# Performance work log

Measured on AMD Instinct MI355X. Metric: run time of the kernel, lower is better.

Reference implementation:

```python
import jax, jax.numpy as jnp
import numpy as np

B, T, D = 4096, 200, 64
N_USERS, N_ITEMS = 100000, 100000


def _linear_init(k, out_dim, in_dim):
    kw, kb = jax.random.split(k)
    lim = 1.0 / np.sqrt(in_dim)
    w = jax.random.uniform(kw, (out_dim, in_dim), minval=-lim, maxval=lim, dtype=jnp.float32)
    b = jax.random.uniform(kb, (out_dim,), minval=-lim, maxval=lim, dtype=jnp.float32)
    return w, b


def setup_inputs() -> dict:
    key = jax.random.key(0)
    ks = jax.random.split(key, 16)
    gru_w_ih, gru_b_ih = _linear_init(ks[0], 3 * D, D)   # torch GRU gate order: r, z, n
    gru_w_hh, gru_b_hh = _linear_init(ks[1], 3 * D, D)
    attn_w, attn_b = _linear_init(ks[2], D, D)
    wr_w, wr_b = _linear_init(ks[3], D, 2 * D)
    wz_w, wz_b = _linear_init(ks[4], D, 2 * D)
    wh_w, wh_b = _linear_init(ks[5], D, 2 * D)
    aux_w, aux_b = _linear_init(ks[6], 1, D)
    item_emb = jax.random.normal(ks[7], (N_ITEMS + 1, D), dtype=jnp.float32)
    user_bias = jax.random.normal(ks[8], (N_USERS, 1), dtype=jnp.float32) * 0.01
    item_bias = jax.random.normal(ks[9], (N_ITEMS, 1), dtype=jnp.float32) * 0.01
    u_idx = jax.random.randint(ks[10], (B,), 0, N_USERS)
    i_idx = jax.random.randint(ks[11], (B,), 0, N_ITEMS)
    seq = jax.random.randint(ks[12], (B, T), 0, N_ITEMS + 1)
    return dict(u_idx=u_idx, i_idx=i_idx, seq=seq,
                item_emb=item_emb, user_bias=user_bias, item_bias=item_bias,
                gru_w_ih=gru_w_ih, gru_b_ih=gru_b_ih, gru_w_hh=gru_w_hh, gru_b_hh=gru_b_hh,
                attn_w=attn_w, attn_b=attn_b,
                wr_w=wr_w, wr_b=wr_b, wz_w=wz_w, wz_b=wz_b, wh_w=wh_w, wh_b=wh_b,
                aux_w=aux_w, aux_b=aux_b)


def _gru(seq_emb, w_ih, b_ih, w_hh, b_hh):
    # seq_emb: [B, T, D]. Precompute input projections for all timesteps.
    x_proj = jnp.einsum('btd,gd->btg', seq_emb, w_ih) + b_ih  # [B, T, 3D]
    x_proj = jnp.transpose(x_proj, (1, 0, 2))                 # [T, B, 3D]
    h0 = jnp.zeros((seq_emb.shape[0], D), dtype=seq_emb.dtype)

    def step(h, xp):
        gh = h @ w_hh.T + b_hh
        xr, xz, xn = jnp.split(xp, 3, axis=-1)
        hr, hz, hn = jnp.split(gh, 3, axis=-1)
        r = jax.nn.sigmoid(xr + hr)
        z = jax.nn.sigmoid(xz + hz)
        n = jnp.tanh(xn + r * hn)
        h_new = (1.0 - z) * n + z * h
        return h_new, h_new

    _, hs = jax.lax.scan(step, h0, x_proj)
    return jnp.transpose(hs, (1, 0, 2))  # [B, T, D]


def _augru(seq_emb, attn_w_t, wr_w, wr_b, wz_w, wz_b, wh_w, wh_b):
    # Split each [D, 2D] weight into x-part and h-part (input was concat([x, h])).
    wr_x, wr_h = wr_w[:, :D], wr_w[:, D:]
    wz_x, wz_h = wz_w[:, :D], wz_w[:, D:]
    wh_x, wh_h = wh_w[:, :D], wh_w[:, D:]
    xr = jnp.einsum('btd,hd->bth', seq_emb, wr_x) + wr_b  # [B, T, D]
    xz = jnp.einsum('btd,hd->bth', seq_emb, wz_x) + wz_b
    xh = jnp.einsum('btd,hd->bth', seq_emb, wh_x) + wh_b
    h0 = jnp.zeros((seq_emb.shape[0], D), dtype=seq_emb.dtype)
    inputs = (jnp.transpose(xr, (1, 0, 2)), jnp.transpose(xz, (1, 0, 2)),
              jnp.transpose(xh, (1, 0, 2)), attn_w_t.T)  # [T,B,D]x3, [T,B]

    def step(h, inp):
        xr_t, xz_t, xh_t, a_t = inp
        r = jax.nn.sigmoid(xr_t + h @ wr_h.T)
        z = jax.nn.sigmoid(xz_t + h @ wz_h.T)
        h_hat = jnp.tanh(xh_t + (r * h) @ wh_h.T)
        z = a_t[:, None] * z
        h_new = (1.0 - z) * h + z * h_hat
        return h_new, None

    h_final, _ = jax.lax.scan(step, h0, inputs)
    return h_final  # [B, D]


def reference(u_idx, i_idx, seq, item_emb, user_bias, item_bias,
              gru_w_ih, gru_b_ih, gru_w_hh, gru_b_hh, attn_w, attn_b,
              wr_w, wr_b, wz_w, wz_b, wh_w, wh_b, aux_w, aux_b):
    fm1 = user_bias[u_idx] + item_bias[i_idx]          # [B, 1]
    target_emb = item_emb[i_idx]                       # [B, D]
    seq_emb = item_emb[seq]                            # [B, T, D]

    gru_out = _gru(seq_emb, gru_w_ih, gru_b_ih, gru_w_hh, gru_b_hh)  # [B, T, D]

    target_proj = target_emb @ attn_w.T + attn_b       # [B, D]
    attn_scores = jnp.einsum('btd,bd->bt', gru_out, target_proj)
    attn_weights = jax.nn.sigmoid(attn_scores)         # [B, T]

    attn_vec = _augru(seq_emb, attn_weights, wr_w, wr_b, wz_w, wz_b, wh_w, wh_b)  # [B, D]

    aux_logits = (gru_out[:, -1, :] @ aux_w.T + aux_b)[:, 0]  # [B]
    return (fm1, attn_vec, aux_logits)
```

## Files before the change

### kernel.cpp

```cpp
#include <hip/hip_runtime.h>

typedef __bf16 bf16x8 __attribute__((ext_vector_type(8)));
typedef float f32x4 __attribute__((ext_vector_type(4)));

#define T_LEN 200
#define NB 4096

__device__ __forceinline__ f32x4 mfma16(bf16x8 a, bf16x8 b, f32x4 c) {
    return __builtin_amdgcn_mfma_f32_16x16x32_bf16(a, b, c, 0, 0, 0);
}
__device__ __forceinline__ float sigf(float x) {
    return __builtin_amdgcn_rcpf(1.0f + __expf(-x));
}
__device__ __forceinline__ float tanh_fast(float x) {
    return 1.0f - 2.0f * __builtin_amdgcn_rcpf(__expf(2.0f * x) + 1.0f);
}

__device__ __forceinline__ unsigned packRNE2(float a, float b) {
    unsigned ha = (unsigned)__builtin_bit_cast(unsigned short, (__bf16)a);
    unsigned hb = (unsigned)__builtin_bit_cast(unsigned short, (__bf16)b);
    return ha | (hb << 16);
}
__device__ __forceinline__ void publish_hi(unsigned short* hp, float v) {
    __bf16 h = (__bf16)v;
    *hp = __builtin_bit_cast(unsigned short, h);
}

struct Frag { bf16x8 hi, lo; };
__device__ __forceinline__ Frag make_frag(f32x4 a, f32x4 b) {
    Frag f;
    #pragma unroll
    for (int j = 0; j < 4; j++) {
        float v = a[j]; __bf16 h = (__bf16)v;
        f.hi[j] = h; f.lo[j] = (__bf16)(v - (float)h);
    }
    #pragma unroll
    for (int j = 0; j < 4; j++) {
        float v = b[j]; __bf16 h = (__bf16)v;
        f.hi[4 + j] = h; f.lo[4 + j] = (__bf16)(v - (float)h);
    }
    return f;
}
__device__ __forceinline__ bf16x8 load_w(const float* p) {
    f32x4 a = *(const f32x4*)p, b = *(const f32x4*)(p + 4);
    bf16x8 w;
    #pragma unroll
    for (int j = 0; j < 4; j++) { w[j] = (__bf16)a[j]; w[4 + j] = (__bf16)b[j]; }
    return w;
}

__global__ __launch_bounds__(512, 2)
void dien_fused(const int* __restrict__ u_idx, const int* __restrict__ i_idx,
                const int* __restrict__ seq, const float* __restrict__ item_emb,
                const float* __restrict__ user_bias, const float* __restrict__ item_bias,
                const float* __restrict__ gw_ih, const float* __restrict__ gb_ih,
                const float* __restrict__ gw_hh, const float* __restrict__ gb_hh,
                const float* __restrict__ attn_w, const float* __restrict__ attn_b,
                const float* __restrict__ wr_w, const float* __restrict__ wr_b,
                const float* __restrict__ wz_w, const float* __restrict__ wz_b,
                const float* __restrict__ wh_w, const float* __restrict__ wh_b,
                const float* __restrict__ aux_w, const float* __restrict__ aux_b,
                float* __restrict__ out)
{
    __shared__ int sSeq[16][T_LEN];
    __shared__ __align__(16) float sTP[16][64];
    __shared__ __align__(16) unsigned short sHGhi[16][72];
    __shared__ __align__(16) unsigned short sHAhi[16][72];
    __shared__ __align__(16) unsigned short sRHhi[16][72];
    __shared__ __align__(16) unsigned short sXhi[16][72];
    __shared__ float sScore[2][16];
    __shared__ float sParts[16][4];

    const int tid  = threadIdx.x;
    const int wave = tid >> 6;
    const int lane = tid & 63;
    const int c    = lane & 15;
    const int q    = lane >> 4;
    const bool isG = (wave < 4);
    const int wg   = wave & 3;
    const int dglob = wg * 16 + c;
    const int row0 = blockIdx.x * 16;

    for (int i = tid; i < 16 * T_LEN; i += 512) {
        int b = i / T_LEN, t = i - b * T_LEN;
        sSeq[b][t] = seq[(row0 + b) * T_LEN + t];
    }

    if (tid < 16) {
        int b = row0 + tid;
        out[b] = user_bias[u_idx[b]] + item_bias[i_idx[b]];
    }

    if (tid < 256) {
        int b  = tid >> 4;
        int d0 = (tid & 15) * 4;
        const float* erow = item_emb + (long)i_idx[row0 + b] * 64;
        float e[64];
        #pragma unroll
        for (int k4 = 0; k4 < 16; k4++) {
            f32x4 v = *(const f32x4*)(erow + k4 * 4);
            #pragma unroll
            for (int j = 0; j < 4; j++) e[k4 * 4 + j] = v[j];
        }
        #pragma unroll
        for (int dd = 0; dd < 4; dd++) {
            int d = d0 + dd;
            const float* wrow = attn_w + d * 64;
            float s = attn_b[d];
            #pragma unroll
            for (int k4 = 0; k4 < 16; k4++) {
                f32x4 wv = *(const f32x4*)(wrow + k4 * 4);
                #pragma unroll
                for (int j = 0; j < 4; j++) s += e[k4 * 4 + j] * wv[j];
            }
            sTP[b][d] = s;
        }
    }

    for (int i = tid; i < 16 * 72; i += 512) sHAhi[0][i] = 0;
    const int xrow = wg * 4 + (lane >> 4);
    const int xch  = lane & 15;
    if (isG) {
        const float* p = item_emb + (long)seq[(row0 + xrow) * T_LEN + 0] * 64 + xch * 4;
        f32x4 v = *(const f32x4*)p;
        *(uint2*)&sXhi[xrow][xch * 4] =
            make_uint2(packRNE2(v[0], v[1]), packRNE2(v[2], v[3]));
    }
    __syncthreads();

    bf16x8 W[12];
    if (isG) {
        #pragma unroll
        for (int g = 0; g < 3; g++)
            #pragma unroll
            for (int s = 0; s < 2; s++) {
                W[g * 2 + s]     = load_w(gw_ih + (g * 64 + dglob) * 64 + s * 32 + q * 8);
                W[6 + g * 2 + s] = load_w(gw_hh + (g * 64 + dglob) * 64 + s * 32 + q * 8);
            }
    } else {
        #pragma unroll
        for (int s = 0; s < 2; s++) {
            const int fo = dglob * 128 + s * 32 + q * 8;
            W[0 + s]  = load_w(wr_w + fo);
            W[2 + s]  = load_w(wr_w + fo + 64);
            W[4 + s]  = load_w(wz_w + fo);
            W[6 + s]  = load_w(wz_w + fo + 64);
            W[8 + s]  = load_w(wh_w + fo);
            W[10 + s] = load_w(wh_w + fo + 64);
        }
    }

    float bA, bB, bC, bD;
    if (isG) {
        bA = gb_ih[dglob] + gb_hh[dglob];
        bB = gb_ih[64 + dglob] + gb_hh[64 + dglob];
        bC = gb_ih[128 + dglob];
        bD = gb_hh[128 + dglob];
    } else {
        bA = wr_b[dglob];
        bB = wz_b[dglob];
        bC = wh_b[dglob];
        bD = 0.0f;
    }
    const float auxwc = aux_w[dglob];

    Frag tpB0, tpB1;
    if (isG) {
        tpB0 = make_frag(*(const f32x4*)&sTP[c][q * 8], *(const f32x4*)&sTP[c][q * 8 + 4]);
        tpB1 = make_frag(*(const f32x4*)&sTP[c][32 + q * 8], *(const f32x4*)&sTP[c][32 + q * 8 + 4]);
    }

    float hst[4] = {0.f, 0.f, 0.f, 0.f};
    bf16x8 fr0, fr1;
    #pragma unroll
    for (int j = 0; j < 8; j++) { fr0[j] = (__bf16)0.f; fr1[j] = (__bf16)0.f; }
    f32x4 aAH = {0.f, 0.f, 0.f, 0.f};
    float z_c[4] = {0.f, 0.f, 0.f, 0.f};

    f32x4 xnxt = {0.f, 0.f, 0.f, 0.f};
    if (isG) {
        int t1 = (T_LEN > 1) ? 1 : 0;
        xnxt = *(const f32x4*)(item_emb + (long)sSeq[xrow][t1] * 64 + xch * 4);
    }

    for (int t = 0; t < T_LEN; t++) {
        f32x4 xg;
        f32x4 aAR, aAZ;

        bf16x8 x0 = *(const bf16x8*)&sXhi[c][q * 8];
        bf16x8 x1 = *(const bf16x8*)&sXhi[c][32 + q * 8];

        if (isG) {
            int tn = t + 2; if (tn > T_LEN - 1) tn = T_LEN - 1;
            xg = *(const f32x4*)(item_emb + (long)sSeq[xrow][tn] * 64 + xch * 4);

            f32x4 accR = {bA, bA, bA, bA};
            accR = mfma16(x0, W[0], accR); accR = mfma16(x1, W[1], accR);
            accR = mfma16(fr0, W[6], accR); accR = mfma16(fr1, W[7], accR);
            f32x4 accZ = {bB, bB, bB, bB};
            accZ = mfma16(x0, W[2], accZ); accZ = mfma16(x1, W[3], accZ);
            accZ = mfma16(fr0, W[8], accZ); accZ = mfma16(fr1, W[9], accZ);
            f32x4 accNX = {bC, bC, bC, bC};
            accNX = mfma16(x0, W[4], accNX); accNX = mfma16(x1, W[5], accNX);
            f32x4 accNH = {bD, bD, bD, bD};
            accNH = mfma16(fr0, W[10], accNH); accNH = mfma16(fr1, W[11], accNH);

            #pragma unroll
            for (int i = 0; i < 4; i++) {
                float r = sigf(accR[i]);
                float z = sigf(accZ[i]);
                float n = tanh_fast(accNX[i] + r * accNH[i]);
                float hn = n + z * (hst[i] - n);
                hst[i] = hn;
                publish_hi(&sHGhi[q * 4 + i][dglob], hn);
            }
        } else {
            if (t > 0) {
                bf16x8 rh0 = *(const bf16x8*)&sRHhi[c][q * 8];
                bf16x8 rh1 = *(const bf16x8*)&sRHhi[c][32 + q * 8];
                aAH = mfma16(rh0, W[10], aAH); aAH = mfma16(rh1, W[11], aAH);
                #pragma unroll
                for (int i = 0; i < 4; i++) {
                    int rr = q * 4 + i;
                    float a = sScore[(t - 1) & 1][rr];
                    float hh = tanh_fast(aAH[i]);
                    float zz = a * z_c[i];
                    float hv = hst[i] + zz * (hh - hst[i]);
                    hst[i] = hv;
                    publish_hi(&sHAhi[rr][dglob], hv);
                }
            }
            aAR = (f32x4){bA, bA, bA, bA};
            aAR = mfma16(x0, W[0], aAR); aAR = mfma16(x1, W[1], aAR);
            aAZ = (f32x4){bB, bB, bB, bB};
            aAZ = mfma16(x0, W[4], aAZ); aAZ = mfma16(x1, W[5], aAZ);
            aAH = (f32x4){bC, bC, bC, bC};
            aAH = mfma16(x0, W[8], aAH); aAH = mfma16(x1, W[9], aAH);
        }

        __syncthreads();

        if (isG) {
            fr0 = *(const bf16x8*)&sHGhi[c][q * 8];
            fr1 = *(const bf16x8*)&sHGhi[c][32 + q * 8];
            f32x4 sc = {0.f, 0.f, 0.f, 0.f};
            sc = mfma16(fr0, tpB0.hi, sc); sc = mfma16(fr0, tpB0.lo, sc);
            sc = mfma16(fr1, tpB1.hi, sc); sc = mfma16(fr1, tpB1.lo, sc);
            if (wg == 0 && (c >> 2) == q) {
                int i = c & 3;
                float d = (i == 0) ? sc[0] : (i == 1) ? sc[1] : (i == 2) ? sc[2] : sc[3];
                sScore[t & 1][c] = sigf(d);
            }
            *(uint2*)&sXhi[xrow][xch * 4] =
                make_uint2(packRNE2(xnxt[0], xnxt[1]), packRNE2(xnxt[2], xnxt[3]));
            xnxt = xg;
        } else {
            bf16x8 ha0 = *(const bf16x8*)&sHAhi[c][q * 8];
            bf16x8 ha1 = *(const bf16x8*)&sHAhi[c][32 + q * 8];
            aAR = mfma16(ha0, W[2], aAR); aAR = mfma16(ha1, W[3], aAR);
            aAZ = mfma16(ha0, W[6], aAZ); aAZ = mfma16(ha1, W[7], aAZ);
            #pragma unroll
            for (int i = 0; i < 4; i++) {
                float r = sigf(aAR[i]);
                z_c[i]  = sigf(aAZ[i]);
                float rh = r * hst[i];
                publish_hi(&sRHhi[q * 4 + i][dglob], rh);
            }
        }

        __syncthreads();
    }

    if (!isG) {
        bf16x8 rh0 = *(const bf16x8*)&sRHhi[c][q * 8];
        bf16x8 rh1 = *(const bf16x8*)&sRHhi[c][32 + q * 8];
        aAH = mfma16(rh0, W[10], aAH); aAH = mfma16(rh1, W[11], aAH);
        #pragma unroll
        for (int i = 0; i < 4; i++) {
            int rr = q * 4 + i;
            float a = sScore[(T_LEN - 1) & 1][rr];
            float hh = tanh_fast(aAH[i]);
            float zz = a * z_c[i];
            float hv = hst[i] + zz * (hh - hst[i]);
            out[NB + (row0 + rr) * 64 + dglob] = hv;
        }
    }

    if (isG) {
        float pa[4];
        #pragma unroll
        for (int i = 0; i < 4; i++) pa[i] = hst[i] * auxwc;
        #pragma unroll
        for (int m = 1; m < 16; m <<= 1) {
            #pragma unroll
            for (int i = 0; i < 4; i++) pa[i] += __shfl_xor(pa[i], m, 64);
        }
        if (c == 0) {
            #pragma unroll
            for (int i = 0; i < 4; i++) sParts[q * 4 + i][wg] = pa[i];
        }
    }
    __syncthreads();
    if (tid < 16) {
        out[NB + NB * 64 + row0 + tid] =
            sParts[tid][0] + sParts[tid][1] + sParts[tid][2] + sParts[tid][3] + aux_b[0];
    }
}

extern "C" void kernel_launch(void* const* d_in, const int* in_sizes, int n_in,
                              void* d_out, int out_size, void* d_ws, size_t ws_size,
                              hipStream_t stream) {
    dien_fused<<<dim3(256), dim3(512), 0, stream>>>(
        (const int*)d_in[0],
        (const int*)d_in[1],
        (const int*)d_in[2],
        (const float*)d_in[3],
        (const float*)d_in[4],
        (const float*)d_in[5],
        (const float*)d_in[6],
        (const float*)d_in[7],
        (const float*)d_in[8],
        (const float*)d_in[9],
        (const float*)d_in[10],
        (const float*)d_in[11],
        (const float*)d_in[12],
        (const float*)d_in[13],
        (const float*)d_in[14],
        (const float*)d_in[15],
        (const float*)d_in[16],
        (const float*)d_in[17],
        (const float*)d_in[18],
        (const float*)d_in[19],
        (float*)d_out);
}
```

Baseline: 263.6 us.

## Move GRU gate math after barrier and compute attention score via shuffle partial sums

The GRU waves now issue their MFMAs before the first barrier but apply the nonlinearities and publish the hidden state after it. The GRU hidden state and input tiles are double-buffered in shared memory. The attention score is no longer an MFMA against a hi/lo split target projection. Each wave instead does fp32 dot-product partials with xor shuffles, writes four per-row partials to shared memory, and the AUGRU waves sum them and apply the sigmoid. This removes the post-barrier reload of h and the 4-MFMA score path from the critical chain, at the cost of extra shuffles and more LDS buffers.

Measured after the change: 331.9 us. 25.9% more time.

```diff
diff --git a/kernel.cpp b/kernel.cpp
--- a/kernel.cpp
+++ b/kernel.cpp
@@ -15,7 +15,6 @@
 __device__ __forceinline__ float tanh_fast(float x) {
     return 1.0f - 2.0f * __builtin_amdgcn_rcpf(__expf(2.0f * x) + 1.0f);
 }
-
 __device__ __forceinline__ unsigned packRNE2(float a, float b) {
     unsigned ha = (unsigned)__builtin_bit_cast(unsigned short, (__bf16)a);
     unsigned hb = (unsigned)__builtin_bit_cast(unsigned short, (__bf16)b);
@@ -24,22 +23,6 @@
 __device__ __forceinline__ void publish_hi(unsigned short* hp, float v) {
     __bf16 h = (__bf16)v;
     *hp = __builtin_bit_cast(unsigned short, h);
-}
-
-struct Frag { bf16x8 hi, lo; };
-__device__ __forceinline__ Frag make_frag(f32x4 a, f32x4 b) {
-    Frag f;
-    #pragma unroll
-    for (int j = 0; j < 4; j++) {
-        float v = a[j]; __bf16 h = (__bf16)v;
-        f.hi[j] = h; f.lo[j] = (__bf16)(v - (float)h);
-    }
-    #pragma unroll
-    for (int j = 0; j < 4; j++) {
-        float v = b[j]; __bf16 h = (__bf16)v;
-        f.hi[4 + j] = h; f.lo[4 + j] = (__bf16)(v - (float)h);
-    }
-    return f;
 }
 __device__ __forceinline__ bf16x8 load_w(const float* p) {
     f32x4 a = *(const f32x4*)p, b = *(const f32x4*)(p + 4);
@@ -64,11 +47,11 @@
 {
     __shared__ int sSeq[16][T_LEN];
     __shared__ __align__(16) float sTP[16][64];
-    __shared__ __align__(16) unsigned short sHGhi[16][72];
-    __shared__ __align__(16) unsigned short sHAhi[16][72];
-    __shared__ __align__(16) unsigned short sRHhi[16][72];
-    __shared__ __align__(16) unsigned short sXhi[16][72];
-    __shared__ float sScore[2][16];
+    __shared__ __align__(16) unsigned short sHG[2][16][72];
+    __shared__ __align__(16) unsigned short sHA[16][72];
+    __shared__ __align__(16) unsigned short sRH[16][72];
+    __shared__ __align__(16) unsigned short sX[2][16][72];
+    __shared__ __align__(16) float sPart[2][16][4];
     __shared__ float sParts[16][4];
 
     const int tid  = threadIdx.x;
@@ -117,13 +100,16 @@
         }
     }
 
-    for (int i = tid; i < 16 * 72; i += 512) sHAhi[0][i] = 0;
-    const int xrow = wg * 4 + (lane >> 4);
-    const int xch  = lane & 15;
+    for (int i = tid; i < 16 * 72; i += 512) {
+        ((unsigned short*)sHA)[i]    = 0;
+        ((unsigned short*)sHG[1])[i] = 0;
+    }
+    const int xrow = wg * 4 + q;
+    const int xch  = c;
     if (isG) {
         const float* p = item_emb + (long)seq[(row0 + xrow) * T_LEN + 0] * 64 + xch * 4;
         f32x4 v = *(const f32x4*)p;
-        *(uint2*)&sXhi[xrow][xch * 4] =
+        *(uint2*)&sX[0][xrow][xch * 4] =
             make_uint2(packRNE2(v[0], v[1]), packRNE2(v[2], v[3]));
     }
     __syncthreads();
@@ -164,47 +150,80 @@
     }
     const float auxwc = aux_w[dglob];
 
-    Frag tpB0, tpB1;
-    if (isG) {
-        tpB0 = make_frag(*(const f32x4*)&sTP[c][q * 8], *(const f32x4*)&sTP[c][q * 8 + 4]);
-        tpB1 = make_frag(*(const f32x4*)&sTP[c][32 + q * 8], *(const f32x4*)&sTP[c][32 + q * 8 + 4]);
+    float tpT[4];
+    if (isG) {
+        #pragma unroll
+        for (int i = 0; i < 4; i++) tpT[i] = sTP[q * 4 + i][dglob];
     }
 
     float hst[4] = {0.f, 0.f, 0.f, 0.f};
-    bf16x8 fr0, fr1;
-    #pragma unroll
-    for (int j = 0; j < 8; j++) { fr0[j] = (__bf16)0.f; fr1[j] = (__bf16)0.f; }
     f32x4 aAH = {0.f, 0.f, 0.f, 0.f};
     float z_c[4] = {0.f, 0.f, 0.f, 0.f};
 
     f32x4 xnxt = {0.f, 0.f, 0.f, 0.f};
-    if (isG) {
-        int t1 = (T_LEN > 1) ? 1 : 0;
-        xnxt = *(const f32x4*)(item_emb + (long)sSeq[xrow][t1] * 64 + xch * 4);
-    }
+    if (isG) xnxt = *(const f32x4*)(item_emb + (long)sSeq[xrow][1] * 64 + xch * 4);
+
+    f32x4 accR, accZ, accNX, accNH;
+    f32x4 aAR, aAZ;
+    f32x4 xg;
 
     for (int t = 0; t < T_LEN; t++) {
-        f32x4 xg;
-        f32x4 aAR, aAZ;
-
-        bf16x8 x0 = *(const bf16x8*)&sXhi[c][q * 8];
-        bf16x8 x1 = *(const bf16x8*)&sXhi[c][32 + q * 8];
-
         if (isG) {
+            bf16x8 x0  = *(const bf16x8*)&sX[t & 1][c][q * 8];
+            bf16x8 x1  = *(const bf16x8*)&sX[t & 1][c][32 + q * 8];
+            bf16x8 fr0 = *(const bf16x8*)&sHG[(t + 1) & 1][c][q * 8];
+            bf16x8 fr1 = *(const bf16x8*)&sHG[(t + 1) & 1][c][32 + q * 8];
+
             int tn = t + 2; if (tn > T_LEN - 1) tn = T_LEN - 1;
             xg = *(const f32x4*)(item_emb + (long)sSeq[xrow][tn] * 64 + xch * 4);
 
-            f32x4 accR = {bA, bA, bA, bA};
+            accR = (f32x4){bA, bA, bA, bA};
             accR = mfma16(x0, W[0], accR); accR = mfma16(x1, W[1], accR);
             accR = mfma16(fr0, W[6], accR); accR = mfma16(fr1, W[7], accR);
-            f32x4 accZ = {bB, bB, bB, bB};
+            accZ = (f32x4){bB, bB, bB, bB};
             accZ = mfma16(x0, W[2], accZ); accZ = mfma16(x1, W[3], accZ);
             accZ = mfma16(fr0, W[8], accZ); accZ = mfma16(fr1, W[9], accZ);
-            f32x4 accNX = {bC, bC, bC, bC};
+            accNX = (f32x4){bC, bC, bC, bC};
             accNX = mfma16(x0, W[4], accNX); accNX = mfma16(x1, W[5], accNX);
-            f32x4 accNH = {bD, bD, bD, bD};
+            accNH = (f32x4){bD, bD, bD, bD};
             accNH = mfma16(fr0, W[10], accNH); accNH = mfma16(fr1, W[11], accNH);
-
+        } else {
+            bf16x8 x0 = *(const bf16x8*)&sX[t & 1][c][q * 8];
+            bf16x8 x1 = *(const bf16x8*)&sX[t & 1][c][32 + q * 8];
+
+            aAR = (f32x4){bA, bA, bA, bA};
+            aAR = mfma16(x0, W[0], aAR); aAR = mfma16(x1, W[1], aAR);
+            aAZ = (f32x4){bB, bB, bB, bB};
+            aAZ = mfma16(x0, W[4], aAZ); aAZ = mfma16(x1, W[5], aAZ);
+
+            if (t > 0) {
+                bf16x8 rh0 = *(const bf16x8*)&sRH[c][q * 8];
+                bf16x8 rh1 = *(const bf16x8*)&sRH[c][32 + q * 8];
+                f32x4 pv0 = *(const f32x4*)&sPart[(t + 1) & 1][q * 4 + 0][0];
+                f32x4 pv1 = *(const f32x4*)&sPart[(t + 1) & 1][q * 4 + 1][0];
+                f32x4 pv2 = *(const f32x4*)&sPart[(t + 1) & 1][q * 4 + 2][0];
+                f32x4 pv3 = *(const f32x4*)&sPart[(t + 1) & 1][q * 4 + 3][0];
+                aAH = mfma16(rh0, W[10], aAH); aAH = mfma16(rh1, W[11], aAH);
+                #pragma unroll
+                for (int i = 0; i < 4; i++) {
+                    int rr = q * 4 + i;
+                    f32x4 pv = (i == 0) ? pv0 : (i == 1) ? pv1 : (i == 2) ? pv2 : pv3;
+                    float a = sigf((pv[0] + pv[1]) + (pv[2] + pv[3]));
+                    float hh = tanh_fast(aAH[i]);
+                    float zz = a * z_c[i];
+                    float hv = hst[i] + zz * (hh - hst[i]);
+                    hst[i] = hv;
+                    publish_hi(&sHA[rr][dglob], hv);
+                }
+            }
+            aAH = (f32x4){bC, bC, bC, bC};
+            aAH = mfma16(x0, W[8], aAH); aAH = mfma16(x1, W[9], aAH);
+        }
+
+        __syncthreads();
+
+        if (isG) {
+            float pa[4];
             #pragma unroll
             for (int i = 0; i < 4; i++) {
                 float r = sigf(accR[i]);
@@ -212,51 +231,24 @@
                 float n = tanh_fast(accNX[i] + r * accNH[i]);
                 float hn = n + z * (hst[i] - n);
                 hst[i] = hn;
-                publish_hi(&sHGhi[q * 4 + i][dglob], hn);
-            }
-        } else {
-            if (t > 0) {
-                bf16x8 rh0 = *(const bf16x8*)&sRHhi[c][q * 8];
-                bf16x8 rh1 = *(const bf16x8*)&sRHhi[c][32 + q * 8];
-                aAH = mfma16(rh0, W[10], aAH); aAH = mfma16(rh1, W[11], aAH);
+                publish_hi(&sHG[t & 1][q * 4 + i][dglob], hn);
+                pa[i] = hn * tpT[i];
+            }
+            #pragma unroll
+            for (int m = 1; m < 16; m <<= 1) {
                 #pragma unroll
-                for (int i = 0; i < 4; i++) {
-                    int rr = q * 4 + i;
-                    float a = sScore[(t - 1) & 1][rr];
-                    float hh = tanh_fast(aAH[i]);
-                    float zz = a * z_c[i];
-                    float hv = hst[i] + zz * (hh - hst[i]);
-                    hst[i] = hv;
-                    publish_hi(&sHAhi[rr][dglob], hv);
-                }
-            }
-            aAR = (f32x4){bA, bA, bA, bA};
-            aAR = mfma16(x0, W[0], aAR); aAR = mfma16(x1, W[1], aAR);
-            aAZ = (f32x4){bB, bB, bB, bB};
-            aAZ = mfma16(x0, W[4], aAZ); aAZ = mfma16(x1, W[5], aAZ);
-            aAH = (f32x4){bC, bC, bC, bC};
-            aAH = mfma16(x0, W[8], aAH); aAH = mfma16(x1, W[9], aAH);
-        }
-
-        __syncthreads();
-
-        if (isG) {
-            fr0 = *(const bf16x8*)&sHGhi[c][q * 8];
-            fr1 = *(const bf16x8*)&sHGhi[c][32 + q * 8];
-            f32x4 sc = {0.f, 0.f, 0.f, 0.f};
-            sc = mfma16(fr0, tpB0.hi, sc); sc = mfma16(fr0, tpB0.lo, sc);
-            sc = mfma16(fr1, tpB1.hi, sc); sc = mfma16(fr1, tpB1.lo, sc);
-            if (wg == 0 && (c >> 2) == q) {
-                int i = c & 3;
-                float d = (i == 0) ? sc[0] : (i == 1) ? sc[1] : (i == 2) ? sc[2] : sc[3];
-                sScore[t & 1][c] = sigf(d);
-            }
-            *(uint2*)&sXhi[xrow][xch * 4] =
+                for (int i = 0; i < 4; i++) pa[i] += __shfl_xor(pa[i], m, 64);
+            }
+            if (c == 0) {
+                #pragma unroll
+                for (int i = 0; i < 4; i++) sPart[t & 1][q * 4 + i][wg] = pa[i];
+            }
+            *(uint2*)&sX[(t + 1) & 1][xrow][xch * 4] =
                 make_uint2(packRNE2(xnxt[0], xnxt[1]), packRNE2(xnxt[2], xnxt[3]));
             xnxt = xg;
         } else {
-            bf16x8 ha0 = *(const bf16x8*)&sHAhi[c][q * 8];
-            bf16x8 ha1 = *(const bf16x8*)&sHAhi[c][32 + q * 8];
+            bf16x8 ha0 = *(const bf16x8*)&sHA[c][q * 8];
+            bf16x8 ha1 = *(const bf16x8*)&sHA[c][32 + q * 8];
             aAR = mfma16(ha0, W[2], aAR); aAR = mfma16(ha1, W[3], aAR);
             aAZ = mfma16(ha0, W[6], aAZ); aAZ = mfma16(ha1, W[7], aAZ);
             #pragma unroll
@@ -264,7 +256,7 @@
                 float r = sigf(aAR[i]);
                 z_c[i]  = sigf(aAZ[i]);
                 float rh = r * hst[i];
-                publish_hi(&sRHhi[q * 4 + i][dglob], rh);
+                publish_hi(&sRH[q * 4 + i][dglob], rh);
             }
         }
 
@@ -272,13 +264,14 @@
     }
 
     if (!isG) {
-        bf16x8 rh0 = *(const bf16x8*)&sRHhi[c][q * 8];
-        bf16x8 rh1 = *(const bf16x8*)&sRHhi[c][32 + q * 8];
+        bf16x8 rh0 = *(const bf16x8*)&sRH[c][q * 8];
+        bf16x8 rh1 = *(const bf16x8*)&sRH[c][32 + q * 8];
         aAH = mfma16(rh0, W[10], aAH); aAH = mfma16(rh1, W[11], aAH);
         #pragma unroll
         for (int i = 0; i < 4; i++) {
             int rr = q * 4 + i;
-            float a = sScore[(T_LEN - 1) & 1][rr];
+            f32x4 pv = *(const f32x4*)&sPart[(T_LEN - 1) & 1][rr][0];
+            float a = sigf((pv[0] + pv[1]) + (pv[2] + pv[3]));
             float hh = tanh_fast(aAH[i]);
             float zz = a * z_c[i];
             float hv = hst[i] + zz * (hh - hst[i]);
```

## Add producer wave group computing input projections one step ahead

Applied to the files above, without the earlier changes.

Adds a third group of four waves (768 threads per block) that computes the GRU and AUGRU input projections and gathers embeddings, writing them into double-buffered shared memory one timestep ahead. The GRU and AUGRU waves then only run their recurrent matmuls, which shortens the serial critical path of each step. In exchange the block is larger and uses more shared memory, and each step still waits on two block-wide barriers across more waves.

New measurement: 304.2 us. +15.4%, slower.

```diff
diff --git a/kernel.cpp b/kernel.cpp
--- a/kernel.cpp
+++ b/kernel.cpp
@@ -15,7 +15,6 @@
 __device__ __forceinline__ float tanh_fast(float x) {
     return 1.0f - 2.0f * __builtin_amdgcn_rcpf(__expf(2.0f * x) + 1.0f);
 }
-
 __device__ __forceinline__ unsigned packRNE2(float a, float b) {
     unsigned ha = (unsigned)__builtin_bit_cast(unsigned short, (__bf16)a);
     unsigned hb = (unsigned)__builtin_bit_cast(unsigned short, (__bf16)b);
@@ -25,7 +24,6 @@
     __bf16 h = (__bf16)v;
     *hp = __builtin_bit_cast(unsigned short, h);
 }
-
 struct Frag { bf16x8 hi, lo; };
 __device__ __forceinline__ Frag make_frag(f32x4 a, f32x4 b) {
     Frag f;
@@ -49,7 +47,7 @@
     return w;
 }
 
-__global__ __launch_bounds__(512, 2)
+__global__ __launch_bounds__(768, 3)
 void dien_fused(const int* __restrict__ u_idx, const int* __restrict__ i_idx,
                 const int* __restrict__ seq, const float* __restrict__ item_emb,
                 const float* __restrict__ user_bias, const float* __restrict__ item_bias,
@@ -68,6 +66,8 @@
     __shared__ __align__(16) unsigned short sHAhi[16][72];
     __shared__ __align__(16) unsigned short sRHhi[16][72];
     __shared__ __align__(16) unsigned short sXhi[16][72];
+    __shared__ __align__(16) float sPG[2][3][64][20];
+    __shared__ __align__(16) float sPA[2][3][64][20];
     __shared__ float sScore[2][16];
     __shared__ float sParts[16][4];
 
@@ -76,12 +76,14 @@
     const int lane = tid & 63;
     const int c    = lane & 15;
     const int q    = lane >> 4;
-    const bool isG = (wave < 4);
+    const int role = wave >> 2;
     const int wg   = wave & 3;
     const int dglob = wg * 16 + c;
     const int row0 = blockIdx.x * 16;
-
-    for (int i = tid; i < 16 * T_LEN; i += 512) {
+    const int xrow = wg * 4 + q;
+    const int xch  = c;
+
+    for (int i = tid; i < 16 * T_LEN; i += 768) {
         int b = i / T_LEN, t = i - b * T_LEN;
         sSeq[b][t] = seq[(row0 + b) * T_LEN + t];
     }
@@ -117,10 +119,8 @@
         }
     }
 
-    for (int i = tid; i < 16 * 72; i += 512) sHAhi[0][i] = 0;
-    const int xrow = wg * 4 + (lane >> 4);
-    const int xch  = lane & 15;
-    if (isG) {
+    for (int i = tid; i < 16 * 72; i += 768) ((unsigned short*)sHAhi)[i] = 0;
+    if (role == 2) {
         const float* p = item_emb + (long)seq[(row0 + xrow) * T_LEN + 0] * 64 + xch * 4;
         f32x4 v = *(const f32x4*)p;
         *(uint2*)&sXhi[xrow][xch * 4] =
@@ -129,46 +129,86 @@
     __syncthreads();
 
     bf16x8 W[12];
-    if (isG) {
+    if (role == 0) {
         #pragma unroll
         for (int g = 0; g < 3; g++)
             #pragma unroll
-            for (int s = 0; s < 2; s++) {
-                W[g * 2 + s]     = load_w(gw_ih + (g * 64 + dglob) * 64 + s * 32 + q * 8);
-                W[6 + g * 2 + s] = load_w(gw_hh + (g * 64 + dglob) * 64 + s * 32 + q * 8);
-            }
+            for (int s = 0; s < 2; s++)
+                W[g * 2 + s] = load_w(gw_hh + (g * 64 + dglob) * 64 + s * 32 + q * 8);
+    } else if (role == 1) {
+        #pragma unroll
+        for (int s = 0; s < 2; s++) {
+            const int fo = dglob * 128 + 64 + s * 32 + q * 8;
+            W[0 + s] = load_w(wr_w + fo);
+            W[2 + s] = load_w(wz_w + fo);
+            W[4 + s] = load_w(wh_w + fo);
+        }
     } else {
+        #pragma unroll
+        for (int g = 0; g < 3; g++)
+            #pragma unroll
+            for (int s = 0; s < 2; s++)
+                W[g * 2 + s] = load_w(gw_ih + (g * 64 + dglob) * 64 + s * 32 + q * 8);
         #pragma unroll
         for (int s = 0; s < 2; s++) {
             const int fo = dglob * 128 + s * 32 + q * 8;
-            W[0 + s]  = load_w(wr_w + fo);
-            W[2 + s]  = load_w(wr_w + fo + 64);
-            W[4 + s]  = load_w(wz_w + fo);
-            W[6 + s]  = load_w(wz_w + fo + 64);
-            W[8 + s]  = load_w(wh_w + fo);
-            W[10 + s] = load_w(wh_w + fo + 64);
-        }
-    }
-
-    float bA, bB, bC, bD;
-    if (isG) {
-        bA = gb_ih[dglob] + gb_hh[dglob];
-        bB = gb_ih[64 + dglob] + gb_hh[64 + dglob];
-        bC = gb_ih[128 + dglob];
+            W[6 + s]  = load_w(wr_w + fo);
+            W[8 + s]  = load_w(wz_w + fo);
+            W[10 + s] = load_w(wh_w + fo);
+        }
+    }
+
+    float bD = 0.f, auxwc = 0.f;
+    float xbA = 0.f, xbB = 0.f, xbC = 0.f, xbR = 0.f, xbZ = 0.f, xbH = 0.f;
+    if (role == 0) {
         bD = gb_hh[128 + dglob];
-    } else {
-        bA = wr_b[dglob];
-        bB = wz_b[dglob];
-        bC = wh_b[dglob];
-        bD = 0.0f;
-    }
-    const float auxwc = aux_w[dglob];
+        auxwc = aux_w[dglob];
+    } else if (role == 2) {
+        xbA = gb_ih[dglob] + gb_hh[dglob];
+        xbB = gb_ih[64 + dglob] + gb_hh[64 + dglob];
+        xbC = gb_ih[128 + dglob];
+        xbR = wr_b[dglob];
+        xbZ = wz_b[dglob];
+        xbH = wh_b[dglob];
+    }
 
     Frag tpB0, tpB1;
-    if (isG) {
+    if (role == 0) {
         tpB0 = make_frag(*(const f32x4*)&sTP[c][q * 8], *(const f32x4*)&sTP[c][q * 8 + 4]);
         tpB1 = make_frag(*(const f32x4*)&sTP[c][32 + q * 8], *(const f32x4*)&sTP[c][32 + q * 8 + 4]);
     }
+
+    f32x4 xn1, xnxt;
+    if (role == 2) {
+        bf16x8 x0 = *(const bf16x8*)&sXhi[c][q * 8];
+        bf16x8 x1 = *(const bf16x8*)&sXhi[c][32 + q * 8];
+        f32x4 a0 = {xbA, xbA, xbA, xbA};
+        a0 = mfma16(x0, W[0], a0); a0 = mfma16(x1, W[1], a0);
+        f32x4 a1 = {xbB, xbB, xbB, xbB};
+        a1 = mfma16(x0, W[2], a1); a1 = mfma16(x1, W[3], a1);
+        f32x4 a2 = {xbC, xbC, xbC, xbC};
+        a2 = mfma16(x0, W[4], a2); a2 = mfma16(x1, W[5], a2);
+        *(f32x4*)&sPG[0][0][dglob][q * 4] = a0;
+        *(f32x4*)&sPG[0][1][dglob][q * 4] = a1;
+        *(f32x4*)&sPG[0][2][dglob][q * 4] = a2;
+        f32x4 a3 = {xbR, xbR, xbR, xbR};
+        a3 = mfma16(x0, W[6], a3); a3 = mfma16(x1, W[7], a3);
+        f32x4 a4 = {xbZ, xbZ, xbZ, xbZ};
+        a4 = mfma16(x0, W[8], a4); a4 = mfma16(x1, W[9], a4);
+        f32x4 a5 = {xbH, xbH, xbH, xbH};
+        a5 = mfma16(x0, W[10], a5); a5 = mfma16(x1, W[11], a5);
+        *(f32x4*)&sPA[0][0][dglob][q * 4] = a3;
+        *(f32x4*)&sPA[0][1][dglob][q * 4] = a4;
+        *(f32x4*)&sPA[0][2][dglob][q * 4] = a5;
+        xn1 = *(const f32x4*)(item_emb + (long)sSeq[xrow][1] * 64 + xch * 4);
+    }
+    __syncthreads();
+    if (role == 2) {
+        *(uint2*)&sXhi[xrow][xch * 4] =
+            make_uint2(packRNE2(xn1[0], xn1[1]), packRNE2(xn1[2], xn1[3]));
+        xnxt = *(const f32x4*)(item_emb + (long)sSeq[xrow][2] * 64 + xch * 4);
+    }
+    __syncthreads();
 
     float hst[4] = {0.f, 0.f, 0.f, 0.f};
     bf16x8 fr0, fr1;
@@ -176,49 +216,36 @@
     for (int j = 0; j < 8; j++) { fr0[j] = (__bf16)0.f; fr1[j] = (__bf16)0.f; }
     f32x4 aAH = {0.f, 0.f, 0.f, 0.f};
     float z_c[4] = {0.f, 0.f, 0.f, 0.f};
-
-    f32x4 xnxt = {0.f, 0.f, 0.f, 0.f};
-    if (isG) {
-        int t1 = (T_LEN > 1) ? 1 : 0;
-        xnxt = *(const f32x4*)(item_emb + (long)sSeq[xrow][t1] * 64 + xch * 4);
-    }
+    f32x4 aAR, aAZ;
+    f32x4 xg;
 
     for (int t = 0; t < T_LEN; t++) {
-        f32x4 xg;
-        f32x4 aAR, aAZ;
-
-        bf16x8 x0 = *(const bf16x8*)&sXhi[c][q * 8];
-        bf16x8 x1 = *(const bf16x8*)&sXhi[c][32 + q * 8];
-
-        if (isG) {
-            int tn = t + 2; if (tn > T_LEN - 1) tn = T_LEN - 1;
-            xg = *(const f32x4*)(item_emb + (long)sSeq[xrow][tn] * 64 + xch * 4);
-
-            f32x4 accR = {bA, bA, bA, bA};
-            accR = mfma16(x0, W[0], accR); accR = mfma16(x1, W[1], accR);
-            accR = mfma16(fr0, W[6], accR); accR = mfma16(fr1, W[7], accR);
-            f32x4 accZ = {bB, bB, bB, bB};
-            accZ = mfma16(x0, W[2], accZ); accZ = mfma16(x1, W[3], accZ);
-            accZ = mfma16(fr0, W[8], accZ); accZ = mfma16(fr1, W[9], accZ);
-            f32x4 accNX = {bC, bC, bC, bC};
-            accNX = mfma16(x0, W[4], accNX); accNX = mfma16(x1, W[5], accNX);
+        const int cur = t & 1, nxt = (t + 1) & 1;
+
+        if (role == 0) {
+            f32x4 pR = *(const f32x4*)&sPG[cur][0][dglob][q * 4];
+            f32x4 pZ = *(const f32x4*)&sPG[cur][1][dglob][q * 4];
+            f32x4 pN = *(const f32x4*)&sPG[cur][2][dglob][q * 4];
+            f32x4 z4 = {0.f, 0.f, 0.f, 0.f};
+            f32x4 accR = mfma16(fr0, W[0], z4);  accR = mfma16(fr1, W[1], accR);
+            f32x4 accZ = mfma16(fr0, W[2], z4);  accZ = mfma16(fr1, W[3], accZ);
             f32x4 accNH = {bD, bD, bD, bD};
-            accNH = mfma16(fr0, W[10], accNH); accNH = mfma16(fr1, W[11], accNH);
-
+            accNH = mfma16(fr0, W[4], accNH); accNH = mfma16(fr1, W[5], accNH);
+            accR += pR; accZ += pZ;
             #pragma unroll
             for (int i = 0; i < 4; i++) {
                 float r = sigf(accR[i]);
                 float z = sigf(accZ[i]);
-                float n = tanh_fast(accNX[i] + r * accNH[i]);
+                float n = tanh_fast(pN[i] + r * accNH[i]);
                 float hn = n + z * (hst[i] - n);
                 hst[i] = hn;
                 publish_hi(&sHGhi[q * 4 + i][dglob], hn);
             }
-        } else {
+        } else if (role == 1) {
             if (t > 0) {
                 bf16x8 rh0 = *(const bf16x8*)&sRHhi[c][q * 8];
                 bf16x8 rh1 = *(const bf16x8*)&sRHhi[c][32 + q * 8];
-                aAH = mfma16(rh0, W[10], aAH); aAH = mfma16(rh1, W[11], aAH);
+                aAH = mfma16(rh0, W[4], aAH); aAH = mfma16(rh1, W[5], aAH);
                 #pragma unroll
                 for (int i = 0; i < 4; i++) {
                     int rr = q * 4 + i;
@@ -230,17 +257,28 @@
                     publish_hi(&sHAhi[rr][dglob], hv);
                 }
             }
-            aAR = (f32x4){bA, bA, bA, bA};
-            aAR = mfma16(x0, W[0], aAR); aAR = mfma16(x1, W[1], aAR);
-            aAZ = (f32x4){bB, bB, bB, bB};
-            aAZ = mfma16(x0, W[4], aAZ); aAZ = mfma16(x1, W[5], aAZ);
-            aAH = (f32x4){bC, bC, bC, bC};
-            aAH = mfma16(x0, W[8], aAH); aAH = mfma16(x1, W[9], aAH);
+            aAR = *(const f32x4*)&sPA[cur][0][dglob][q * 4];
+            aAZ = *(const f32x4*)&sPA[cur][1][dglob][q * 4];
+            aAH = *(const f32x4*)&sPA[cur][2][dglob][q * 4];
+        } else {
+            fr0 = *(const bf16x8*)&sXhi[c][q * 8];
+            fr1 = *(const bf16x8*)&sXhi[c][32 + q * 8];
+            int tn = t + 3; if (tn > T_LEN - 1) tn = T_LEN - 1;
+            xg = *(const f32x4*)(item_emb + (long)sSeq[xrow][tn] * 64 + xch * 4);
+            f32x4 a0 = {xbA, xbA, xbA, xbA};
+            a0 = mfma16(fr0, W[0], a0); a0 = mfma16(fr1, W[1], a0);
+            f32x4 a1 = {xbB, xbB, xbB, xbB};
+            a1 = mfma16(fr0, W[2], a1); a1 = mfma16(fr1, W[3], a1);
+            f32x4 a2 = {xbC, xbC, xbC, xbC};
+            a2 = mfma16(fr0, W[4], a2); a2 = mfma16(fr1, W[5], a2);
+            *(f32x4*)&sPG[nxt][0][dglob][q * 4] = a0;
+            *(f32x4*)&sPG[nxt][1][dglob][q * 4] = a1;
+            *(f32x4*)&sPG[nxt][2][dglob][q * 4] = a2;
         }
 
         __syncthreads();
 
-        if (isG) {
+        if (role == 0) {
             fr0 = *(const bf16x8*)&sHGhi[c][q * 8];
             fr1 = *(const bf16x8*)&sHGhi[c][32 + q * 8];
             f32x4 sc = {0.f, 0.f, 0.f, 0.f};
@@ -249,16 +287,13 @@
             if (wg == 0 && (c >> 2) == q) {
                 int i = c & 3;
                 float d = (i == 0) ? sc[0] : (i == 1) ? sc[1] : (i == 2) ? sc[2] : sc[3];
-                sScore[t & 1][c] = sigf(d);
-            }
-            *(uint2*)&sXhi[xrow][xch * 4] =
-                make_uint2(packRNE2(xnxt[0], xnxt[1]), packRNE2(xnxt[2], xnxt[3]));
-            xnxt = xg;
-        } else {
+                sScore[cur][c] = sigf(d);
+            }
+        } else if (role == 1) {
             bf16x8 ha0 = *(const bf16x8*)&sHAhi[c][q * 8];
             bf16x8 ha1 = *(const bf16x8*)&sHAhi[c][32 + q * 8];
-            aAR = mfma16(ha0, W[2], aAR); aAR = mfma16(ha1, W[3], aAR);
-            aAZ = mfma16(ha0, W[6], aAZ); aAZ = mfma16(ha1, W[7], aAZ);
+            aAR = mfma16(ha0, W[0], aAR); aAR = mfma16(ha1, W[1], aAR);
+            aAZ = mfma16(ha0, W[2], aAZ); aAZ = mfma16(ha1, W[3], aAZ);
             #pragma unroll
             for (int i = 0; i < 4; i++) {
                 float r = sigf(aAR[i]);
@@ -266,15 +301,28 @@
                 float rh = r * hst[i];
                 publish_hi(&sRHhi[q * 4 + i][dglob], rh);
             }
+        } else {
+            f32x4 a3 = {xbR, xbR, xbR, xbR};
+            a3 = mfma16(fr0, W[6], a3); a3 = mfma16(fr1, W[7], a3);
+            f32x4 a4 = {xbZ, xbZ, xbZ, xbZ};
+            a4 = mfma16(fr0, W[8], a4); a4 = mfma16(fr1, W[9], a4);
+            f32x4 a5 = {xbH, xbH, xbH, xbH};
+            a5 = mfma16(fr0, W[10], a5); a5 = mfma16(fr1, W[11], a5);
+            *(f32x4*)&sPA[nxt][0][dglob][q * 4] = a3;
+            *(f32x4*)&sPA[nxt][1][dglob][q * 4] = a4;
+            *(f32x4*)&sPA[nxt][2][dglob][q * 4] = a5;
+            *(uint2*)&sXhi[xrow][xch * 4] =
+                make_uint2(packRNE2(xnxt[0], xnxt[1]), packRNE2(xnxt[2], xnxt[3]));
+            xnxt = xg;
         }
 
         __syncthreads();
     }
 
-    if (!isG) {
+    if (role == 1) {
         bf16x8 rh0 = *(const bf16x8*)&sRHhi[c][q * 8];
         bf16x8 rh1 = *(const bf16x8*)&sRHhi[c][32 + q * 8];
-        aAH = mfma16(rh0, W[10], aAH); aAH = mfma16(rh1, W[11], aAH);
+        aAH = mfma16(rh0, W[4], aAH); aAH = mfma16(rh1, W[5], aAH);
         #pragma unroll
         for (int i = 0; i < 4; i++) {
             int rr = q * 4 + i;
@@ -286,7 +334,7 @@
         }
     }
 
-    if (isG) {
+    if (role == 0) {
         float pa[4];
         #pragma unroll
         for (int i = 0; i < 4; i++) pa[i] = hst[i] * auxwc;
@@ -310,7 +358,7 @@
 extern "C" void kernel_launch(void* const* d_in, const int* in_sizes, int n_in,
                               void* d_out, int out_size, void* d_ws, size_t ws_size,
                               hipStream_t stream) {
-    dien_fused<<<dim3(256), dim3(512), 0, stream>>>(
+    dien_fused<<<dim3(256), dim3(768), 0, stream>>>(
         (const int*)d_in[0],
         (const int*)d_in[1],
         (const int*)d_in[2],
```

## Transpose MFMA operand order so each lane owns four contiguous hidden dims

Applied to the files above, without the earlier changes.

Swaps the A/B operands of every gate MFMA so the accumulator layout is transposed. Each lane now holds four consecutive hidden units for one batch row, which allows packed 8-byte bf16 stores of the hidden state instead of four scalar 2-byte LDS stores. It also allows vectorized bias loads, a vectorized f32x4 output store and a shorter aux reduction. The attention-score MFMAs are restricted to wave 0, so the three other GRU waves no longer compute them redundantly. The risk is subtle index errors in the new layout, though the row and column mappings look consistent.

Result: slower. 272.2 us (+3.3%).

```diff
diff --git a/kernel.cpp b/kernel.cpp
--- a/kernel.cpp
+++ b/kernel.cpp
@@ -15,17 +15,11 @@
 __device__ __forceinline__ float tanh_fast(float x) {
     return 1.0f - 2.0f * __builtin_amdgcn_rcpf(__expf(2.0f * x) + 1.0f);
 }
-
 __device__ __forceinline__ unsigned packRNE2(float a, float b) {
     unsigned ha = (unsigned)__builtin_bit_cast(unsigned short, (__bf16)a);
     unsigned hb = (unsigned)__builtin_bit_cast(unsigned short, (__bf16)b);
     return ha | (hb << 16);
 }
-__device__ __forceinline__ void publish_hi(unsigned short* hp, float v) {
-    __bf16 h = (__bf16)v;
-    *hp = __builtin_bit_cast(unsigned short, h);
-}
-
 struct Frag { bf16x8 hi, lo; };
 __device__ __forceinline__ Frag make_frag(f32x4 a, f32x4 b) {
     Frag f;
@@ -79,6 +73,7 @@
     const bool isG = (wave < 4);
     const int wg   = wave & 3;
     const int dglob = wg * 16 + c;
+    const int dbase = wg * 16 + q * 4;
     const int row0 = blockIdx.x * 16;
 
     for (int i = tid; i < 16 * T_LEN; i += 512) {
@@ -118,8 +113,8 @@
     }
 
     for (int i = tid; i < 16 * 72; i += 512) sHAhi[0][i] = 0;
-    const int xrow = wg * 4 + (lane >> 4);
-    const int xch  = lane & 15;
+    const int xrow = wg * 4 + q;
+    const int xch  = c;
     if (isG) {
         const float* p = item_emb + (long)seq[(row0 + xrow) * T_LEN + 0] * 64 + xch * 4;
         f32x4 v = *(const f32x4*)p;
@@ -150,19 +145,18 @@
         }
     }
 
-    float bA, bB, bC, bD;
-    if (isG) {
-        bA = gb_ih[dglob] + gb_hh[dglob];
-        bB = gb_ih[64 + dglob] + gb_hh[64 + dglob];
-        bC = gb_ih[128 + dglob];
-        bD = gb_hh[128 + dglob];
+    f32x4 bA4, bB4, bC4, bD4;
+    if (isG) {
+        bA4 = *(const f32x4*)(gb_ih + dbase)       + *(const f32x4*)(gb_hh + dbase);
+        bB4 = *(const f32x4*)(gb_ih + 64 + dbase)  + *(const f32x4*)(gb_hh + 64 + dbase);
+        bC4 = *(const f32x4*)(gb_ih + 128 + dbase);
+        bD4 = *(const f32x4*)(gb_hh + 128 + dbase);
     } else {
-        bA = wr_b[dglob];
-        bB = wz_b[dglob];
-        bC = wh_b[dglob];
-        bD = 0.0f;
-    }
-    const float auxwc = aux_w[dglob];
+        bA4 = *(const f32x4*)(wr_b + dbase);
+        bB4 = *(const f32x4*)(wz_b + dbase);
+        bC4 = *(const f32x4*)(wh_b + dbase);
+        bD4 = (f32x4){0.f, 0.f, 0.f, 0.f};
+    }
 
     Frag tpB0, tpB1;
     if (isG) {
@@ -178,10 +172,7 @@
     float z_c[4] = {0.f, 0.f, 0.f, 0.f};
 
     f32x4 xnxt = {0.f, 0.f, 0.f, 0.f};
-    if (isG) {
-        int t1 = (T_LEN > 1) ? 1 : 0;
-        xnxt = *(const f32x4*)(item_emb + (long)sSeq[xrow][t1] * 64 + xch * 4);
-    }
+    if (isG) xnxt = *(const f32x4*)(item_emb + (long)sSeq[xrow][1] * 64 + xch * 4);
 
     for (int t = 0; t < T_LEN; t++) {
         f32x4 xg;
@@ -194,48 +185,51 @@
             int tn = t + 2; if (tn > T_LEN - 1) tn = T_LEN - 1;
             xg = *(const f32x4*)(item_emb + (long)sSeq[xrow][tn] * 64 + xch * 4);
 
-            f32x4 accR = {bA, bA, bA, bA};
-            accR = mfma16(x0, W[0], accR); accR = mfma16(x1, W[1], accR);
-            accR = mfma16(fr0, W[6], accR); accR = mfma16(fr1, W[7], accR);
-            f32x4 accZ = {bB, bB, bB, bB};
-            accZ = mfma16(x0, W[2], accZ); accZ = mfma16(x1, W[3], accZ);
-            accZ = mfma16(fr0, W[8], accZ); accZ = mfma16(fr1, W[9], accZ);
-            f32x4 accNX = {bC, bC, bC, bC};
-            accNX = mfma16(x0, W[4], accNX); accNX = mfma16(x1, W[5], accNX);
-            f32x4 accNH = {bD, bD, bD, bD};
-            accNH = mfma16(fr0, W[10], accNH); accNH = mfma16(fr1, W[11], accNH);
-
+            f32x4 accR = bA4;
+            accR = mfma16(W[0], x0, accR); accR = mfma16(W[1], x1, accR);
+            accR = mfma16(W[6], fr0, accR); accR = mfma16(W[7], fr1, accR);
+            f32x4 accZ = bB4;
+            accZ = mfma16(W[2], x0, accZ); accZ = mfma16(W[3], x1, accZ);
+            accZ = mfma16(W[8], fr0, accZ); accZ = mfma16(W[9], fr1, accZ);
+            f32x4 accNX = bC4;
+            accNX = mfma16(W[4], x0, accNX); accNX = mfma16(W[5], x1, accNX);
+            f32x4 accNH = bD4;
+            accNH = mfma16(W[10], fr0, accNH); accNH = mfma16(W[11], fr1, accNH);
+
+            float hn[4];
             #pragma unroll
             for (int i = 0; i < 4; i++) {
                 float r = sigf(accR[i]);
                 float z = sigf(accZ[i]);
                 float n = tanh_fast(accNX[i] + r * accNH[i]);
-                float hn = n + z * (hst[i] - n);
-                hst[i] = hn;
-                publish_hi(&sHGhi[q * 4 + i][dglob], hn);
-            }
+                hn[i] = n + z * (hst[i] - n);
+                hst[i] = hn[i];
+            }
+            *(uint2*)&sHGhi[c][dbase] =
+                make_uint2(packRNE2(hn[0], hn[1]), packRNE2(hn[2], hn[3]));
         } else {
             if (t > 0) {
                 bf16x8 rh0 = *(const bf16x8*)&sRHhi[c][q * 8];
                 bf16x8 rh1 = *(const bf16x8*)&sRHhi[c][32 + q * 8];
-                aAH = mfma16(rh0, W[10], aAH); aAH = mfma16(rh1, W[11], aAH);
+                aAH = mfma16(W[10], rh0, aAH); aAH = mfma16(W[11], rh1, aAH);
+                float a = sScore[(t - 1) & 1][c];
+                float hv[4];
                 #pragma unroll
                 for (int i = 0; i < 4; i++) {
-                    int rr = q * 4 + i;
-                    float a = sScore[(t - 1) & 1][rr];
                     float hh = tanh_fast(aAH[i]);
                     float zz = a * z_c[i];
-                    float hv = hst[i] + zz * (hh - hst[i]);
-                    hst[i] = hv;
-                    publish_hi(&sHAhi[rr][dglob], hv);
+                    hv[i] = hst[i] + zz * (hh - hst[i]);
+                    hst[i] = hv[i];
                 }
-            }
-            aAR = (f32x4){bA, bA, bA, bA};
-            aAR = mfma16(x0, W[0], aAR); aAR = mfma16(x1, W[1], aAR);
-            aAZ = (f32x4){bB, bB, bB, bB};
-            aAZ = mfma16(x0, W[4], aAZ); aAZ = mfma16(x1, W[5], aAZ);
-            aAH = (f32x4){bC, bC, bC, bC};
-            aAH = mfma16(x0, W[8], aAH); aAH = mfma16(x1, W[9], aAH);
+                *(uint2*)&sHAhi[c][dbase] =
+                    make_uint2(packRNE2(hv[0], hv[1]), packRNE2(hv[2], hv[3]));
+            }
+            aAR = bA4;
+            aAR = mfma16(W[0], x0, aAR); aAR = mfma16(W[1], x1, aAR);
+            aAZ = bB4;
+            aAZ = mfma16(W[4], x0, aAZ); aAZ = mfma16(W[5], x1, aAZ);
+            aAH = bC4;
+            aAH = mfma16(W[8], x0, aAH); aAH = mfma16(W[9], x1, aAH);
         }
 
         __syncthreads();
@@ -243,13 +237,15 @@
         if (isG) {
             fr0 = *(const bf16x8*)&sHGhi[c][q * 8];
             fr1 = *(const bf16x8*)&sHGhi[c][32 + q * 8];
-            f32x4 sc = {0.f, 0.f, 0.f, 0.f};
-            sc = mfma16(fr0, tpB0.hi, sc); sc = mfma16(fr0, tpB0.lo, sc);
-            sc = mfma16(fr1, tpB1.hi, sc); sc = mfma16(fr1, tpB1.lo, sc);
-            if (wg == 0 && (c >> 2) == q) {
-                int i = c & 3;
-                float d = (i == 0) ? sc[0] : (i == 1) ? sc[1] : (i == 2) ? sc[2] : sc[3];
-                sScore[t & 1][c] = sigf(d);
+            if (wg == 0) {
+                f32x4 sc = {0.f, 0.f, 0.f, 0.f};
+                sc = mfma16(fr0, tpB0.hi, sc); sc = mfma16(fr0, tpB0.lo, sc);
+                sc = mfma16(fr1, tpB1.hi, sc); sc = mfma16(fr1, tpB1.lo, sc);
+                if ((c >> 2) == q) {
+                    int i = c & 3;
+                    float d = (i == 0) ? sc[0] : (i == 1) ? sc[1] : (i == 2) ? sc[2] : sc[3];
+                    sScore[t & 1][c] = sigf(d);
+                }
             }
             *(uint2*)&sXhi[xrow][xch * 4] =
                 make_uint2(packRNE2(xnxt[0], xnxt[1]), packRNE2(xnxt[2], xnxt[3]));
@@ -257,15 +253,17 @@
         } else {
             bf16x8 ha0 = *(const bf16x8*)&sHAhi[c][q * 8];
             bf16x8 ha1 = *(const bf16x8*)&sHAhi[c][32 + q * 8];
-            aAR = mfma16(ha0, W[2], aAR); aAR = mfma16(ha1, W[3], aAR);
-            aAZ = mfma16(ha0, W[6], aAZ); aAZ = mfma16(ha1, W[7], aAZ);
+            aAR = mfma16(W[2], ha0, aAR); aAR = mfma16(W[3], ha1, aAR);
+            aAZ = mfma16(W[6], ha0, aAZ); aAZ = mfma16(W[7], ha1, aAZ);
+            float rh[4];
             #pragma unroll
             for (int i = 0; i < 4; i++) {
                 float r = sigf(aAR[i]);
                 z_c[i]  = sigf(aAZ[i]);
-                float rh = r * hst[i];
-                publish_hi(&sRHhi[q * 4 + i][dglob], rh);
-            }
+                rh[i]   = r * hst[i];
+            }
+            *(uint2*)&sRHhi[c][dbase] =
+                make_uint2(packRNE2(rh[0], rh[1]), packRNE2(rh[2], rh[3]));
         }
 
         __syncthreads();
@@ -274,31 +272,25 @@
     if (!isG) {
         bf16x8 rh0 = *(const bf16x8*)&sRHhi[c][q * 8];
         bf16x8 rh1 = *(const bf16x8*)&sRHhi[c][32 + q * 8];
-        aAH = mfma16(rh0, W[10], aAH); aAH = mfma16(rh1, W[11], aAH);
+        aAH = mfma16(W[10], rh0, aAH); aAH = mfma16(W[11], rh1, aAH);
+        float a = sScore[(T_LEN - 1) & 1][c];
+        f32x4 hv;
         #pragma unroll
         for (int i = 0; i < 4; i++) {
-            int rr = q * 4 + i;
-            float a = sScore[(T_LEN - 1) & 1][rr];
             float hh = tanh_fast(aAH[i]);
             float zz = a * z_c[i];
-            float hv = hst[i] + zz * (hh - hst[i]);
-            out[NB + (row0 + rr) * 64 + dglob] = hv;
-        }
-    }
-
-    if (isG) {
-        float pa[4];
-        #pragma unroll
-        for (int i = 0; i < 4; i++) pa[i] = hst[i] * auxwc;
-        #pragma unroll
-        for (int m = 1; m < 16; m <<= 1) {
-            #pragma unroll
-            for (int i = 0; i < 4; i++) pa[i] += __shfl_xor(pa[i], m, 64);
-        }
-        if (c == 0) {
-            #pragma unroll
-            for (int i = 0; i < 4; i++) sParts[q * 4 + i][wg] = pa[i];
-        }
+            hv[i] = hst[i] + zz * (hh - hst[i]);
+        }
+        *(f32x4*)(out + NB + (long)(row0 + c) * 64 + dbase) = hv;
+    }
+
+    if (isG) {
+        f32x4 auxw4 = *(const f32x4*)(aux_w + dbase);
+        float pa = hst[0] * auxw4[0] + hst[1] * auxw4[1]
+                 + hst[2] * auxw4[2] + hst[3] * auxw4[3];
+        pa += __shfl_xor(pa, 16, 64);
+        pa += __shfl_xor(pa, 32, 64);
+        if (q == 0) sParts[c][wg] = pa;
     }
     __syncthreads();
     if (tid < 16) {
```
